# Performance work log

Hardware: AMD Instinct MI355X
Metric: run time of the kernel (lower is better)

## Reference

```python
import jax, jax.numpy as jnp
import numpy as np
import math

SIZE = (60, 270, 480)           # full video T, H, W
CHANNELS = 14                   # sum of per-level grid channels 8+4+2
GRID_SIZES = [(60, 16, 16, 8), (30, 8, 8, 4), (15, 4, 4, 2)]
IDX_MAX = (60, 3, 5)            # patch grid -> patch_size (1, 90, 96)
PADDING = (0, 1, 1)
N_PATCH = 64
MANIP_LBASE = 2.0
MANIP_LEVELS = 8
INIT_SCALE = 1e-3


def setup_inputs() -> dict:
    key = jax.random.key(0)
    kt, kh, kw = jax.random.split(key, 3)
    idx = jnp.stack([
        jax.random.randint(kt, (N_PATCH,), 0, IDX_MAX[0]),
        jax.random.randint(kh, (N_PATCH,), 0, IDX_MAX[1]),
        jax.random.randint(kw, (N_PATCH,), 0, IDX_MAX[2]),
    ], axis=1).astype(jnp.int32)
    inp = {
        "idx": idx,
        "idx_max": jnp.asarray(IDX_MAX, dtype=jnp.int32),
        "padding": jnp.asarray(PADDING, dtype=jnp.int32),
    }
    for i, (T, H, W, C) in enumerate(GRID_SIZES):
        k = jax.random.fold_in(key, 10 + i)
        inp[f"grid{i}"] = jax.random.normal(k, (T * H * W, C), jnp.float32) * INIT_SCALE
    return inp


def _pixel_idx_1d(ix, size_d, nmax_d, pad_d):
    # ix: [N] patch index along one dim -> ([N, P+2*pad] clipped pixel idx, mask)
    p = size_d // nmax_d
    offs = jnp.arange(-pad_d, p + pad_d)
    raw = ix[:, None] * p + offs[None, :]
    mask = ((raw >= 0) & (raw < size_d)).astype(jnp.float32)
    return jnp.clip(raw, 0, size_d - 1), mask


def reference(idx, idx_max, padding, grid0, grid1, grid2):
    T, H, W = SIZE
    im = tuple(int(v) for v in np.asarray(idx_max))
    pad = tuple(int(v) for v in np.asarray(padding))
    patch = tuple(SIZE[d] // im[d] for d in range(3))
    ppad = tuple(patch[d] + 2 * pad[d] for d in range(3))

    # Multi-level grids -> trilinear upsample to full (T,H,W,C_i), concat on C.
    # jax.image.resize 'trilinear' uses half-pixel centers == torch align_corners=False.
    enc_splits = []
    for g, (Tg, Hg, Wg, Cg) in zip((grid0, grid1, grid2), GRID_SIZES):
        enc_splits.append(jax.image.resize(g.reshape(Tg, Hg, Wg, Cg), (T, H, W, Cg), method="trilinear"))
    enc = jnp.concatenate(enc_splits, axis=-1).reshape(T * H * W, CHANNELS)

    it, mt = _pixel_idx_1d(idx[:, 0], T, im[0], pad[0])
    ih, mh = _pixel_idx_1d(idx[:, 1], H, im[1], pad[1])
    iw, mw = _pixel_idx_1d(idx[:, 2], W, im[2], pad[2])

    flat = (it[:, :, None, None] * (H * W) + ih[:, None, :, None] * W + iw[:, None, None, :]).reshape(-1)
    mask = (mt[:, :, None, None] * mh[:, None, :, None] * mw[:, None, None, :]).reshape(-1, 1)

    t_embed = (mask * enc[flat]).reshape((idx.shape[0],) + ppad + (CHANNELS,))

    bases = (MANIP_LBASE ** jnp.arange(MANIP_LEVELS, dtype=jnp.float32)) * math.pi
    v = idx[:, 0].astype(jnp.float32)[:, None] * bases
    t_manip = jnp.concatenate([jnp.sin(v), jnp.cos(v)], axis=-1)  # [N, 2*levels]

    return t_embed, t_manip
```

## Files before the change

### kernel.cpp

```cpp
#include <hip/hip_runtime.h>
#include <math.h>


#define N_PATCH 64
#define PPAD_H 92
#define PPAD_W 98
#define CH 14
#define PIX_PER_PATCH (PPAD_H * PPAD_W)
#define F2_PER_PATCH (PIX_PER_PATCH * CH / 2)
#define BLOCKS_PER_PATCH 28
#define SLICE (F2_PER_PATCH / BLOCKS_PER_PATCH)
#define TOTAL_EMBED (N_PATCH * PIX_PER_PATCH * CH)
#define TOTAL_MANIP (N_PATCH * 16)

#define L1_BASE 2048
#define L2_BASE 2304

__device__ __forceinline__ float lerpf(float a, float b, float f) {
    return a + f * (b - a);
}

__global__ __launch_bounds__(256) void embed_kernel(
    const int* __restrict__ idx,
    const float* __restrict__ g0,
    const float* __restrict__ g1,
    const float* __restrict__ g2,
    float* __restrict__ out)
{
    __shared__ float  s_grid[2336];
    __shared__ float4 s_hl[3][PPAD_H];
    __shared__ float4 s_wl[3][PPAD_W];

    const int tid = threadIdx.x;
    const int n   = blockIdx.y;
    const int it  = idx[3 * n + 0];
    const int ih  = idx[3 * n + 1];
    const int iw  = idx[3 * n + 2];

    {
        const float4* src = (const float4*)(g0 + (size_t)it * 2048);
        float4* dst = (float4*)s_grid;
        for (int i = tid; i < 512; i += 256) dst[i] = src[i];
    }
    {
        float xt = ((float)it + 0.5f) * 0.5f - 0.5f;
        float ftf = floorf(xt);
        float ft  = xt - ftf;
        int t0 = (int)ftf;
        int t0c = min(max(t0, 0), 29), t1c = min(t0 + 1, 29);
        const float* p0 = g1 + t0c * 256;
        const float* p1 = g1 + t1c * 256;
        if (tid < 256) s_grid[L1_BASE + tid] = lerpf(p0[tid], p1[tid], ft);
    }
    {
        float xt = ((float)it + 0.5f) * 0.25f - 0.5f;
        float ftf = floorf(xt);
        float ft  = xt - ftf;
        int t0 = (int)ftf;
        int t0c = min(max(t0, 0), 14), t1c = min(t0 + 1, 14);
        const float* p0 = g2 + t0c * 32;
        const float* p1 = g2 + t1c * 32;
        if (tid < 32) s_grid[L2_BASE + tid] = lerpf(p0[tid], p1[tid], ft);
    }
    if (tid < PPAD_H) {
        int rh = ih * 90 + tid - 1;
        float ok = ((unsigned)rh < 270u) ? 1.0f : 0.0f;
        const int   Hgs[3] = {16, 8, 4};
        const int   rst[3] = {16 * 8, 8 * 4, 4 * 2};
        const float shs[3] = {(float)((double)16 / 270.0),
                              (float)((double)8  / 270.0),
                              (float)((double)4  / 270.0)};
        #pragma unroll
        for (int l = 0; l < 3; ++l) {
            float xh = ((float)rh + 0.5f) * shs[l] - 0.5f;
            float ff = floorf(xh);
            float f  = xh - ff;
            int h0 = (int)ff;
            int h0c = min(max(h0, 0), Hgs[l] - 1);
            int h1c = min(h0 + 1, Hgs[l] - 1);
            s_hl[l][tid] = make_float4(__int_as_float(h0c * rst[l]),
                                       __int_as_float(h1c * rst[l]), f, ok);
        }
    }
    if (tid < PPAD_W) {
        int rw = iw * 96 + tid - 1;
        float ok = ((unsigned)rw < 480u) ? 1.0f : 0.0f;
        const int   Wgs[3] = {16, 8, 4};
        const int   cst[3] = {8, 4, 2};
        const float sws[3] = {(float)((double)16 / 480.0),
                              (float)((double)8  / 480.0),
                              (float)((double)4  / 480.0)};
        #pragma unroll
        for (int l = 0; l < 3; ++l) {
            float xw = ((float)rw + 0.5f) * sws[l] - 0.5f;
            float ff = floorf(xw);
            float f  = xw - ff;
            int w0 = (int)ff;
            int w0c = min(max(w0, 0), Wgs[l] - 1);
            int w1c = min(w0 + 1, Wgs[l] - 1);
            s_wl[l][tid] = make_float4(__int_as_float(w0c * cst[l]),
                                       __int_as_float(w1c * cst[l]), f, ok);
        }
    }

    if (blockIdx.x == 0 && n == 0) {
        float* om = out + TOTAL_EMBED;
        for (int e = tid; e < TOTAL_MANIP; e += 256) {
            int nn = e >> 4;
            int j  = e & 15;
            int l  = j & 7;
            float base = (float)M_PI * (float)(1 << l);
            float v = (float)idx[3 * nn + 0] * base;
            double dv = (double)v;
            om[e] = (float)((j < 8) ? sin(dv) : cos(dv));
        }
    }

    __syncthreads();

    const int lj0 = blockIdx.x * SLICE;
    const int ljend = lj0 + SLICE;
    float2* o = ((float2*)out) + (size_t)n * F2_PER_PATCH;

    for (int lj = lj0 + tid; lj < ljend; lj += 256) {
        unsigned p = (unsigned)lj / 7u;
        int q = lj - 7 * (int)p;
        unsigned hh = p / 98u;
        int ww = (int)p - 98 * (int)hh;

        int lvl = (q >= 4) + (q >= 6);
        int cb = 2 * q;
        if (lvl == 1) cb = L1_BASE - 8 + 2 * q;
        if (lvl == 2) cb = L2_BASE;

        float4 hl = s_hl[lvl][hh];
        float4 wl = s_wl[lvl][ww];
        int ho0 = __float_as_int(hl.x), ho1 = __float_as_int(hl.y);
        int wo0 = __float_as_int(wl.x), wo1 = __float_as_int(wl.y);
        float fh = hl.z, fw = wl.z;
        float mm = hl.w * wl.w;

        const float* gb = s_grid + cb;
        float2 a = *(const float2*)(gb + ho0 + wo0);
        float2 b = *(const float2*)(gb + ho0 + wo1);
        float2 c = *(const float2*)(gb + ho1 + wo0);
        float2 d = *(const float2*)(gb + ho1 + wo1);

        float2 r;
        r.x = mm * lerpf(lerpf(a.x, b.x, fw), lerpf(c.x, d.x, fw), fh);
        r.y = mm * lerpf(lerpf(a.y, b.y, fw), lerpf(c.y, d.y, fw), fh);
        o[lj] = r;
    }
}

extern "C" void kernel_launch(void* const* d_in, const int* in_sizes, int n_in,
                              void* d_out, int out_size, void* d_ws, size_t ws_size,
                              hipStream_t stream) {
    const int*   idx = (const int*)  d_in[0];
    const float* g0  = (const float*)d_in[3];
    const float* g1  = (const float*)d_in[4];
    const float* g2  = (const float*)d_in[5];
    float* out = (float*)d_out;

    dim3 grid(BLOCKS_PER_PATCH, N_PATCH);
    embed_kernel<<<grid, 256, 0, stream>>>(idx, g0, g1, g2, out);
}
```

Measured before the change: 15.53 us.

## Precompute H/T-interpolated row values per two-row block and stage outputs in LDS

Each block now covers two output rows. It first interpolates the grids along T and H for just the cells those rows touch, into a small shared array. After that each pixel only needs a W-direction lerp on float4 shared loads, and results go through a shared buffer so the global store is one coalesced float4 write. This removes the full per-frame grid staging and the per-element 4-tap bilinear with integer div/mod. The cost is an extra barrier, 46 blocks per patch instead of 28, and about 60 idle threads during the compute phase.

```diff
diff --git a/kernel.cpp b/kernel.cpp
--- a/kernel.cpp
+++ b/kernel.cpp
@@ -7,17 +7,27 @@
 #define PPAD_W 98
 #define CH 14
 #define PIX_PER_PATCH (PPAD_H * PPAD_W)
-#define F2_PER_PATCH (PIX_PER_PATCH * CH / 2)
-#define BLOCKS_PER_PATCH 28
-#define SLICE (F2_PER_PATCH / BLOCKS_PER_PATCH)
-#define TOTAL_EMBED (N_PATCH * PIX_PER_PATCH * CH)
+#define ROWS_PER_BLOCK 2
+#define BLOCKS_PER_PATCH 46
+#define PX_PER_BLOCK 196
+#define F4_PER_BLOCK (PX_PER_BLOCK * CH / 4)
+#define ELEMS_PER_PATCH (PIX_PER_PATCH * CH)
+#define ELEMS_PER_BLOCK (PX_PER_BLOCK * CH)
+#define TOTAL_EMBED (N_PATCH * ELEMS_PER_PATCH)
 #define TOTAL_MANIP (N_PATCH * 16)
 
-#define L1_BASE 2048
-#define L2_BASE 2304
+#define RB_STRIDE 72
+#define L1_OFF 48
+#define L2_OFF 64
 
 __device__ __forceinline__ float lerpf(float a, float b, float f) {
     return a + f * (b - a);
+}
+
+__device__ __forceinline__ int wcell0(int rw0, float sw, int Wg) {
+    float x = ((float)rw0 + 0.5f) * sw - 0.5f;
+    int w0 = (int)floorf(x);
+    return min(max(w0, 0), Wg - 1);
 }
 
 __global__ __launch_bounds__(256) void embed_kernel(
@@ -27,83 +37,26 @@
     const float* __restrict__ g2,
     float* __restrict__ out)
 {
-    __shared__ float  s_grid[2336];
-    __shared__ float4 s_hl[3][PPAD_H];
+    __shared__ __align__(16) float s_V[ROWS_PER_BLOCK * RB_STRIDE];
     __shared__ float4 s_wl[3][PPAD_W];
+    __shared__ __align__(16) float s_buf[PX_PER_BLOCK * CH];
 
     const int tid = threadIdx.x;
+    const int bx  = blockIdx.x;
     const int n   = blockIdx.y;
     const int it  = idx[3 * n + 0];
     const int ih  = idx[3 * n + 1];
     const int iw  = idx[3 * n + 2];
-
-    {
-        const float4* src = (const float4*)(g0 + (size_t)it * 2048);
-        float4* dst = (float4*)s_grid;
-        for (int i = tid; i < 512; i += 256) dst[i] = src[i];
-    }
-    {
-        float xt = ((float)it + 0.5f) * 0.5f - 0.5f;
-        float ftf = floorf(xt);
-        float ft  = xt - ftf;
-        int t0 = (int)ftf;
-        int t0c = min(max(t0, 0), 29), t1c = min(t0 + 1, 29);
-        const float* p0 = g1 + t0c * 256;
-        const float* p1 = g1 + t1c * 256;
-        if (tid < 256) s_grid[L1_BASE + tid] = lerpf(p0[tid], p1[tid], ft);
-    }
-    {
-        float xt = ((float)it + 0.5f) * 0.25f - 0.5f;
-        float ftf = floorf(xt);
-        float ft  = xt - ftf;
-        int t0 = (int)ftf;
-        int t0c = min(max(t0, 0), 14), t1c = min(t0 + 1, 14);
-        const float* p0 = g2 + t0c * 32;
-        const float* p1 = g2 + t1c * 32;
-        if (tid < 32) s_grid[L2_BASE + tid] = lerpf(p0[tid], p1[tid], ft);
-    }
-    if (tid < PPAD_H) {
-        int rh = ih * 90 + tid - 1;
-        float ok = ((unsigned)rh < 270u) ? 1.0f : 0.0f;
-        const int   Hgs[3] = {16, 8, 4};
-        const int   rst[3] = {16 * 8, 8 * 4, 4 * 2};
-        const float shs[3] = {(float)((double)16 / 270.0),
-                              (float)((double)8  / 270.0),
-                              (float)((double)4  / 270.0)};
-        #pragma unroll
-        for (int l = 0; l < 3; ++l) {
-            float xh = ((float)rh + 0.5f) * shs[l] - 0.5f;
-            float ff = floorf(xh);
-            float f  = xh - ff;
-            int h0 = (int)ff;
-            int h0c = min(max(h0, 0), Hgs[l] - 1);
-            int h1c = min(h0 + 1, Hgs[l] - 1);
-            s_hl[l][tid] = make_float4(__int_as_float(h0c * rst[l]),
-                                       __int_as_float(h1c * rst[l]), f, ok);
-        }
-    }
-    if (tid < PPAD_W) {
-        int rw = iw * 96 + tid - 1;
-        float ok = ((unsigned)rw < 480u) ? 1.0f : 0.0f;
-        const int   Wgs[3] = {16, 8, 4};
-        const int   cst[3] = {8, 4, 2};
-        const float sws[3] = {(float)((double)16 / 480.0),
-                              (float)((double)8  / 480.0),
-                              (float)((double)4  / 480.0)};
-        #pragma unroll
-        for (int l = 0; l < 3; ++l) {
-            float xw = ((float)rw + 0.5f) * sws[l] - 0.5f;
-            float ff = floorf(xw);
-            float f  = xw - ff;
-            int w0 = (int)ff;
-            int w0c = min(max(w0, 0), Wgs[l] - 1);
-            int w1c = min(w0 + 1, Wgs[l] - 1);
-            s_wl[l][tid] = make_float4(__int_as_float(w0c * cst[l]),
-                                       __int_as_float(w1c * cst[l]), f, ok);
-        }
-    }
-
-    if (blockIdx.x == 0 && n == 0) {
+    const int rw0 = iw * 96 - 1;
+
+    const float sw0 = (float)((double)16 / 480.0);
+    const float sw1 = (float)((double)8  / 480.0);
+    const float sw2 = (float)((double)4  / 480.0);
+    const float sh0 = (float)((double)16 / 270.0);
+    const float sh1 = (float)((double)8  / 270.0);
+    const float sh2 = (float)((double)4  / 270.0);
+
+    if (bx == 0 && n == 0) {
         float* om = out + TOTAL_EMBED;
         for (int e = tid; e < TOTAL_MANIP; e += 256) {
             int nn = e >> 4;
@@ -116,41 +69,155 @@
         }
     }
 
+    if (tid < 96) {
+        int chn  = tid & 7;
+        int u    = tid >> 3;
+        int row  = (u >= 6);
+        int cell = u - 6 * row;
+        int rh   = ih * 90 + (bx * 2 + row) - 1;
+        float mh = ((unsigned)rh < 270u) ? 1.0f : 0.0f;
+        float xh = ((float)rh + 0.5f) * sh0 - 0.5f;
+        float ff = floorf(xh);
+        float fh = xh - ff;
+        int h0 = (int)ff;
+        int h0c = min(max(h0, 0), 15), h1c = min(h0 + 1, 15);
+        int cw = min(wcell0(rw0, sw0, 16) + cell, 15);
+        const float* base = g0 + (size_t)it * 2048;
+        float a = base[(h0c * 16 + cw) * 8 + chn];
+        float b = base[(h1c * 16 + cw) * 8 + chn];
+        s_V[row * RB_STRIDE + cell * 8 + chn] = mh * lerpf(a, b, fh);
+    } else if (tid < 128) {
+        int i    = tid - 96;
+        int chn  = i & 3;
+        int u    = i >> 2;
+        int row  = (u >= 4);
+        int cell = u - 4 * row;
+        int rh   = ih * 90 + (bx * 2 + row) - 1;
+        float mh = ((unsigned)rh < 270u) ? 1.0f : 0.0f;
+        float xh = ((float)rh + 0.5f) * sh1 - 0.5f;
+        float ff = floorf(xh);
+        float fh = xh - ff;
+        int h0 = (int)ff;
+        int h0c = min(max(h0, 0), 7), h1c = min(h0 + 1, 7);
+        float xt = ((float)it + 0.5f) * 0.5f - 0.5f;
+        float ftf = floorf(xt);
+        float ft  = xt - ftf;
+        int t0 = (int)ftf;
+        int t0c = min(max(t0, 0), 29), t1c = min(t0 + 1, 29);
+        int cw = min(wcell0(rw0, sw1, 8) + cell, 7);
+        float a00 = g1[((t0c * 8 + h0c) * 8 + cw) * 4 + chn];
+        float a01 = g1[((t0c * 8 + h1c) * 8 + cw) * 4 + chn];
+        float a10 = g1[((t1c * 8 + h0c) * 8 + cw) * 4 + chn];
+        float a11 = g1[((t1c * 8 + h1c) * 8 + cw) * 4 + chn];
+        s_V[row * RB_STRIDE + L1_OFF + cell * 4 + chn] =
+            mh * lerpf(lerpf(a00, a01, fh), lerpf(a10, a11, fh), ft);
+    } else if (tid < 140) {
+        int i    = tid - 128;
+        int chn  = i & 1;
+        int u    = i >> 1;
+        int row  = (u >= 3);
+        int cell = u - 3 * row;
+        int rh   = ih * 90 + (bx * 2 + row) - 1;
+        float mh = ((unsigned)rh < 270u) ? 1.0f : 0.0f;
+        float xh = ((float)rh + 0.5f) * sh2 - 0.5f;
+        float ff = floorf(xh);
+        float fh = xh - ff;
+        int h0 = (int)ff;
+        int h0c = min(max(h0, 0), 3), h1c = min(h0 + 1, 3);
+        float xt = ((float)it + 0.5f) * 0.25f - 0.5f;
+        float ftf = floorf(xt);
+        float ft  = xt - ftf;
+        int t0 = (int)ftf;
+        int t0c = min(max(t0, 0), 14), t1c = min(t0 + 1, 14);
+        int cw = min(wcell0(rw0, sw2, 4) + cell, 3);
+        float a00 = g2[((t0c * 4 + h0c) * 4 + cw) * 2 + chn];
+        float a01 = g2[((t0c * 4 + h1c) * 4 + cw) * 2 + chn];
+        float a10 = g2[((t1c * 4 + h0c) * 4 + cw) * 2 + chn];
+        float a11 = g2[((t1c * 4 + h1c) * 4 + cw) * 2 + chn];
+        s_V[row * RB_STRIDE + L2_OFF + cell * 2 + chn] =
+            mh * lerpf(lerpf(a00, a01, fh), lerpf(a10, a11, fh), ft);
+    }
+
+    for (int i = tid; i < 3 * PPAD_W; i += 256) {
+        int lvl = (i >= PPAD_W) + (i >= 2 * PPAD_W);
+        int ww  = i - PPAD_W * lvl;
+        int Wg  = (lvl == 0) ? 16 : ((lvl == 1) ? 8 : 4);
+        int cs  = (lvl == 0) ? 8  : ((lvl == 1) ? 4 : 2);
+        int bb  = (lvl == 0) ? 0  : ((lvl == 1) ? L1_OFF : L2_OFF);
+        float sw = (lvl == 0) ? sw0 : ((lvl == 1) ? sw1 : sw2);
+        int rw = iw * 96 + ww - 1;
+        float mask = ((unsigned)rw < 480u) ? 1.0f : 0.0f;
+        float x  = ((float)rw + 0.5f) * sw - 0.5f;
+        float ff = floorf(x);
+        float f  = x - ff;
+        int w0 = (int)ff;
+        int wa = min(max(w0, 0), Wg - 1);
+        int wb = min(w0 + 1, Wg - 1);
+        int C0 = wcell0(rw0, sw, Wg);
+        s_wl[lvl][ww] = make_float4(__int_as_float(bb + (wa - C0) * cs),
+                                    __int_as_float(bb + (wb - C0) * cs), f, mask);
+    }
+
     __syncthreads();
 
-    const int lj0 = blockIdx.x * SLICE;
-    const int ljend = lj0 + SLICE;
-    float2* o = ((float2*)out) + (size_t)n * F2_PER_PATCH;
-
-    for (int lj = lj0 + tid; lj < ljend; lj += 256) {
-        unsigned p = (unsigned)lj / 7u;
-        int q = lj - 7 * (int)p;
-        unsigned hh = p / 98u;
-        int ww = (int)p - 98 * (int)hh;
-
-        int lvl = (q >= 4) + (q >= 6);
-        int cb = 2 * q;
-        if (lvl == 1) cb = L1_BASE - 8 + 2 * q;
-        if (lvl == 2) cb = L2_BASE;
-
-        float4 hl = s_hl[lvl][hh];
-        float4 wl = s_wl[lvl][ww];
-        int ho0 = __float_as_int(hl.x), ho1 = __float_as_int(hl.y);
-        int wo0 = __float_as_int(wl.x), wo1 = __float_as_int(wl.y);
-        float fh = hl.z, fw = wl.z;
-        float mm = hl.w * wl.w;
-
-        const float* gb = s_grid + cb;
-        float2 a = *(const float2*)(gb + ho0 + wo0);
-        float2 b = *(const float2*)(gb + ho0 + wo1);
-        float2 c = *(const float2*)(gb + ho1 + wo0);
-        float2 d = *(const float2*)(gb + ho1 + wo1);
-
-        float2 r;
-        r.x = mm * lerpf(lerpf(a.x, b.x, fw), lerpf(c.x, d.x, fw), fh);
-        r.y = mm * lerpf(lerpf(a.y, b.y, fw), lerpf(c.y, d.y, fw), fh);
-        o[lj] = r;
-    }
+    if (tid < PX_PER_BLOCK) {
+        int row = (tid >= PPAD_W);
+        int ww  = tid - PPAD_W * row;
+        const float* V = s_V + row * RB_STRIDE;
+        float r[CH];
+
+        float4 wl0 = s_wl[0][ww];
+        {
+            int oA = __float_as_int(wl0.x), oB = __float_as_int(wl0.y);
+            float fw = wl0.z;
+            float4 A0 = *(const float4*)(V + oA);
+            float4 A1 = *(const float4*)(V + oA + 4);
+            float4 B0 = *(const float4*)(V + oB);
+            float4 B1 = *(const float4*)(V + oB + 4);
+            r[0] = lerpf(A0.x, B0.x, fw);
+            r[1] = lerpf(A0.y, B0.y, fw);
+            r[2] = lerpf(A0.z, B0.z, fw);
+            r[3] = lerpf(A0.w, B0.w, fw);
+            r[4] = lerpf(A1.x, B1.x, fw);
+            r[5] = lerpf(A1.y, B1.y, fw);
+            r[6] = lerpf(A1.z, B1.z, fw);
+            r[7] = lerpf(A1.w, B1.w, fw);
+        }
+        {
+            float4 wl1 = s_wl[1][ww];
+            int oA = __float_as_int(wl1.x), oB = __float_as_int(wl1.y);
+            float fw = wl1.z;
+            float4 A = *(const float4*)(V + oA);
+            float4 B = *(const float4*)(V + oB);
+            r[8]  = lerpf(A.x, B.x, fw);
+            r[9]  = lerpf(A.y, B.y, fw);
+            r[10] = lerpf(A.z, B.z, fw);
+            r[11] = lerpf(A.w, B.w, fw);
+        }
+        {
+            float4 wl2 = s_wl[2][ww];
+            int oA = __float_as_int(wl2.x), oB = __float_as_int(wl2.y);
+            float fw = wl2.z;
+            float2 A = *(const float2*)(V + oA);
+            float2 B = *(const float2*)(V + oB);
+            r[12] = lerpf(A.x, B.x, fw);
+            r[13] = lerpf(A.y, B.y, fw);
+        }
+        float mw = wl0.w;
+        float2* b = (float2*)(s_buf + tid * CH);
+        b[0] = make_float2(mw * r[0],  mw * r[1]);
+        b[1] = make_float2(mw * r[2],  mw * r[3]);
+        b[2] = make_float2(mw * r[4],  mw * r[5]);
+        b[3] = make_float2(mw * r[6],  mw * r[7]);
+        b[4] = make_float2(mw * r[8],  mw * r[9]);
+        b[5] = make_float2(mw * r[10], mw * r[11]);
+        b[6] = make_float2(mw * r[12], mw * r[13]);
+    }
+    __syncthreads();
+
+    const float4* sb = (const float4*)s_buf;
+    float4* gb = (float4*)(out + (size_t)n * ELEMS_PER_PATCH + bx * ELEMS_PER_BLOCK);
+    for (int j = tid; j < F4_PER_BLOCK; j += 256) gb[j] = sb[j];
 }
 
 extern "C" void kernel_launch(void* const* d_in, const int* in_sizes, int n_in,
```

Measured after the change: 12.76 us. -17.9%, faster.
